# Kernel optimization log

Measured on AMD Instinct MI355X. Metric: run time of the kernel, lower is better.

The kernel has to match this reference:

```python
import jax, jax.numpy as jnp
import numpy as np

B, S, D, H, L = 16, 1024, 512, 8, 32
DH = D // H  # 64


def setup_inputs() -> dict:
    key = jax.random.key(0)
    ks = jax.random.split(key, 12)
    p = lambda k, shape: 0.02 * jax.random.normal(k, shape, jnp.float32)
    return {
        "e_all": jax.random.normal(ks[0], (B, S, D), jnp.float32),
        "e_last": jax.random.normal(ks[1], (1, B, D), jnp.float32),
        "target": jax.random.normal(ks[2], (B, L, 3), jnp.float32),
        "Wq": p(ks[3], (D, D)), "bq": jnp.zeros((D,), jnp.float32),
        "Wk": p(ks[4], (D, D)), "bk": jnp.zeros((D,), jnp.float32),
        "Wv": p(ks[5], (D, D)), "bv": jnp.zeros((D,), jnp.float32),
        "Wo": p(ks[6], (D, D)), "bo": jnp.zeros((D,), jnp.float32),
        "W_ih": p(ks[7], (3 * D, 3 + D)), "W_hh": p(ks[8], (3 * D, D)),
        "b_ih": jnp.zeros((3 * D,), jnp.float32), "b_hh": jnp.zeros((3 * D,), jnp.float32),
        "W_out": p(ks[9], (3, D)), "b_out": jnp.zeros((3,), jnp.float32),
    }


def _forward(e_all, e_last, target, Wq, bq, Wk, bk, Wv, bv, Wo, bo,
             W_ih, W_hh, b_ih, b_hh, W_out, b_out):
    # K/V projections over e_all are loop-invariant in the original python loop;
    # hoist them (identical math). NOTE: the original reshape(B, H, S, DH) on a
    # [B, S, D] tensor is a plain row-major reshape (not a head split) -- kept faithful.
    K = (e_all @ Wk.T + bk).reshape(B, H, S, DH)
    V = (e_all @ Wv.T + bv).reshape(B, H, S, DH)
    h0 = e_last[0]  # [B, D] (single-layer GRU hidden)
    # teacher forcing: step 0 sees zeros, step i sees target[:, i-1]
    d_inputs = jnp.concatenate(
        [jnp.zeros((B, 1, 3), jnp.float32), target[:, :L - 1]], axis=1
    ).transpose(1, 0, 2)  # [L, B, 3]

    def step(h, d_in):
        q = (h @ Wq.T + bq).reshape(B, H, 1, DH)
        # faithful scaling quirk: dim_head ** 1 / 2 == DH / 2
        scores = jnp.einsum('bhqd,bhkd->bhqk', q, K) / (DH / 2)
        dist = jax.nn.softmax(scores, axis=-1)            # [B, H, 1, S]
        attn = jnp.einsum('bhqk,bhkd->bhqd', dist, V).reshape(B, D)
        attn = attn @ Wo.T + bo                           # out projection
        x = jnp.concatenate([attn, d_in], axis=-1)        # [B, D+3]
        gi = x @ W_ih.T + b_ih
        gh = h @ W_hh.T + b_hh
        i_r, i_z, i_n = jnp.split(gi, 3, axis=-1)
        h_r, h_z, h_n = jnp.split(gh, 3, axis=-1)
        r = jax.nn.sigmoid(i_r + h_r)
        z = jax.nn.sigmoid(i_z + h_z)
        n = jnp.tanh(i_n + r * h_n)
        h_new = (1 - z) * n + z * h
        out = h_new @ W_out.T + b_out                     # [B, 3]
        return h_new, (out, dist[:, :, 0, :])

    h_fin, (outs, dists) = jax.lax.scan(step, h0, d_inputs)
    d_outputs = outs.transpose(1, 0, 2)        # [B, L, 3]
    cross_attn = dists.transpose(1, 2, 0, 3)   # [B, H, L, S]
    return d_outputs, h_fin[None, :, :], cross_attn


def reference(e_all, e_last, target, Wq, bq, Wk, bk, Wv, bv, Wo, bo,
              W_ih, W_hh, b_ih, b_hh, W_out, b_out):
    return _forward(e_all, e_last, target, Wq, bq, Wk, bk, Wv, bv, Wo, bo,
                    W_ih, W_hh, b_ih, b_hh, W_out, b_out)
```

## Files before the change

### kernel.cpp

```cpp
#include <hip/hip_runtime.h>
#include <hip/hip_bf16.h>
#include <cstdint>

#define B_  16
#define S_  1024
#define D_  512
#define H_  8
#define L_  32
#define DH_ 64

typedef __attribute__((ext_vector_type(8))) short bf16x8;
typedef __attribute__((ext_vector_type(4))) float f32x4;

__device__ __forceinline__ float bf2f(unsigned short u) {
    union { unsigned int u; float f; } x; x.u = ((unsigned int)u) << 16; return x.f;
}
__device__ __forceinline__ unsigned short f2bf(float f) {
    union { float f; unsigned int u; } x; x.f = f;
    unsigned int r = x.u + 0x7fffu + ((x.u >> 16) & 1u);
    return (unsigned short)(r >> 16);
}

__device__ __forceinline__ void st_dev(float* p, float v) {
    __hip_atomic_store(p, v, __ATOMIC_RELAXED, __HIP_MEMORY_SCOPE_AGENT);
}
__device__ __forceinline__ float ld_dev(const float* p) {
    return __hip_atomic_load(p, __ATOMIC_RELAXED, __HIP_MEMORY_SCOPE_AGENT);
}


__global__ void k_conv(const float* __restrict__ in, unsigned short* __restrict__ out, int n) {
    int i = (blockIdx.x * 256 + threadIdx.x) * 4;
    int stride = gridDim.x * 1024;
    for (; i < n; i += stride) {
        float4 v = *reinterpret_cast<const float4*>(in + i);
        out[i + 0] = f2bf(v.x); out[i + 1] = f2bf(v.y);
        out[i + 2] = f2bf(v.z); out[i + 3] = f2bf(v.w);
    }
}

__global__ void k_transpose_bf(const float* __restrict__ in, unsigned short* __restrict__ out,
                               int R, int C) {
    __shared__ float tile[32][33];
    int c0 = blockIdx.x * 32, r0 = blockIdx.y * 32;
    int tx = threadIdx.x, ty = threadIdx.y;
#pragma unroll
    for (int i = 0; i < 4; i++)
        tile[ty + i * 8][tx] = in[(size_t)(r0 + ty + i * 8) * C + c0 + tx];
    __syncthreads();
#pragma unroll
    for (int i = 0; i < 4; i++)
        out[(size_t)(c0 + ty + i * 8) * R + r0 + tx] = f2bf(tile[tx][ty + i * 8]);
}

__global__ void k_conv_wih(const float* __restrict__ in, unsigned short* __restrict__ out) {
    int i = blockIdx.x * 256 + threadIdx.x;
    int j = i >> 9, k = i & 511;
    out[i] = f2bf(in[j * 515 + k]);
}

__global__ void k_bf_wd(const float* __restrict__ Wih, const float* __restrict__ bih,
                        const float* __restrict__ bo, float* __restrict__ bf_,
                        float* __restrict__ Wd) {
    int j = blockIdx.x * 256 + threadIdx.x;
    if (j >= 1536) return;
    float acc = bih[j];
    for (int k = 0; k < 512; k++) acc += Wih[(size_t)j * 515 + k] * bo[k];
    bf_[j] = acc;
    Wd[j * 3 + 0] = Wih[(size_t)j * 515 + 512];
    Wd[j * 3 + 1] = Wih[(size_t)j * 515 + 513];
    Wd[j * 3 + 2] = Wih[(size_t)j * 515 + 514];
}

__global__ void k_dterm2(const float* __restrict__ target, const float* __restrict__ Wd,
                         const float* __restrict__ bf_, const float* __restrict__ bhh,
                         float* __restrict__ gacc) {
    int i = blockIdx.x * 256 + threadIdx.x;
    int j = i % 3072; int bl = i / 3072; int b = bl % 16; int l = bl / 16;
    float acc;
    if (j < 1536) {
        acc = bf_[j];
        if (l > 0) {
            const float* tg = target + ((size_t)b * L_ + (l - 1)) * 3;
            acc += tg[0] * Wd[j * 3 + 0] + tg[1] * Wd[j * 3 + 1] + tg[2] * Wd[j * 3 + 2];
        }
    } else {
        acc = bhh[j - 1536];
    }
    gacc[i] = acc;
}

template <bool BF16OUT>
__global__ __launch_bounds__(256) void k_gemm_bt(
    const unsigned short* __restrict__ A, const unsigned short* __restrict__ Bm,
    void* __restrict__ Cout, const float* __restrict__ bias, int M, int N, int Kd) {
    __shared__ unsigned short As[128 * 64];
    __shared__ unsigned short Bs[128 * 64];
    const int t = threadIdx.x;
    const int lane = t & 63;
    const int w = t >> 6, wr = w >> 1, wc = w & 1;
    const int m0 = blockIdx.x * 128, n0 = blockIdx.y * 128;
    f32x4 acc[4][4];
#pragma unroll
    for (int i = 0; i < 4; i++)
#pragma unroll
        for (int j = 0; j < 4; j++) acc[i][j] = (f32x4){0.f, 0.f, 0.f, 0.f};

    const int rowt = t >> 3, colt = (t & 7) * 8;
    for (int k0 = 0; k0 < Kd; k0 += 64) {
#pragma unroll
        for (int i = 0; i < 4; i++) {
            int row = i * 32 + rowt;
            __builtin_amdgcn_global_load_lds(
                (const __attribute__((address_space(1))) unsigned int*)(A + (size_t)(m0 + row) * Kd + k0 + colt),
                (__attribute__((address_space(3))) unsigned int*)(As + (i * 256 + t) * 8), 16, 0, 0);
            __builtin_amdgcn_global_load_lds(
                (const __attribute__((address_space(1))) unsigned int*)(Bm + (size_t)(n0 + row) * Kd + k0 + colt),
                (__attribute__((address_space(3))) unsigned int*)(Bs + (i * 256 + t) * 8), 16, 0, 0);
        }
        asm volatile("s_waitcnt vmcnt(0)" ::: "memory");
        __syncthreads();
#pragma unroll
        for (int kk = 0; kk < 2; kk++) {
            bf16x8 af[4], bfr[4];
#pragma unroll
            for (int mi = 0; mi < 4; mi++)
                af[mi] = *reinterpret_cast<const bf16x8*>(
                    As + (wr * 64 + mi * 16 + (lane & 15)) * 64 + kk * 32 + (lane >> 4) * 8);
#pragma unroll
            for (int ni = 0; ni < 4; ni++)
                bfr[ni] = *reinterpret_cast<const bf16x8*>(
                    Bs + (wc * 64 + ni * 16 + (lane & 15)) * 64 + kk * 32 + (lane >> 4) * 8);
#pragma unroll
            for (int mi = 0; mi < 4; mi++)
#pragma unroll
                for (int ni = 0; ni < 4; ni++)
                    acc[mi][ni] = __builtin_amdgcn_mfma_f32_16x16x32_bf16(af[mi], bfr[ni], acc[mi][ni], 0, 0, 0);
        }
        __syncthreads();
    }
    const int rr = (lane >> 4) * 4, cc = lane & 15;
#pragma unroll
    for (int mi = 0; mi < 4; mi++) {
#pragma unroll
        for (int ni = 0; ni < 4; ni++) {
            int col = n0 + wc * 64 + ni * 16 + cc;
            float bv = bias ? bias[col] : 0.f;
            int rowb = m0 + wr * 64 + mi * 16 + rr;
#pragma unroll
            for (int r = 0; r < 4; r++) {
                float v = acc[mi][ni][r] + bv;
                if (BF16OUT) ((unsigned short*)Cout)[(size_t)(rowb + r) * N + col] = f2bf(v);
                else         ((float*)Cout)[(size_t)(rowb + r) * N + col] = v;
            }
        }
    }
}

__device__ __forceinline__ void group_barrier(unsigned* bar, unsigned tgt) {
    asm volatile("s_waitcnt vmcnt(0)" ::: "memory");
    __syncthreads();
    if (threadIdx.x == 0) {
        __hip_atomic_fetch_add(bar, 1u, __ATOMIC_RELAXED, __HIP_MEMORY_SCOPE_AGENT);
        while (__hip_atomic_load(bar, __ATOMIC_RELAXED, __HIP_MEMORY_SCOPE_AGENT) < tgt)
            __builtin_amdgcn_s_sleep(1);
    }
    __syncthreads();
}

__global__ __launch_bounds__(1024, 1) void k_decode(
    const unsigned short* __restrict__ K16, const unsigned short* __restrict__ V16,
    const unsigned short* __restrict__ Wq16, const float* __restrict__ bq,
    const unsigned short* __restrict__ WfT16, const unsigned short* __restrict__ WhhT16,
    float* __restrict__ gacc, float* __restrict__ ssx, const float* __restrict__ e_last,
    const float* __restrict__ Wout, const float* __restrict__ bout,
    float* __restrict__ dout, float* __restrict__ hfin, float* __restrict__ cross,
    unsigned* __restrict__ bars) {
    const int t = threadIdx.x, lane = t & 63, w = t >> 6;
    const int bi = blockIdx.x >> 4, hd = (blockIdx.x >> 1) & 7, sh = blockIdx.x & 1;

    __shared__ char Ks[65536];
    __shared__ char Vs[65536];
    __shared__ float hsh[512];
    __shared__ float qsh[64];
    __shared__ float esh[512];
    __shared__ float red[1024];
    __shared__ float pvred[1024];
    __shared__ float ash[64];
    __shared__ float wred[32];
    __shared__ float sh_ssinv;

    const size_t base = (size_t)bi * (S_ * D_) + (size_t)hd * (S_ * DH_) + (size_t)sh * (512 * 64);

    {
        const int row = t >> 1, half = t & 1;
        const unsigned short* kr = K16 + base + (size_t)row * 64 + half * 32;
        const unsigned short* vr = V16 + base + (size_t)row * 64 + half * 32;
        char* krow = Ks + row * 128;
        char* vrow = Vs + row * 128;
#pragma unroll
        for (int c = 0; c < 4; c++) {
            int slot = half * 4 + c;
            *reinterpret_cast<bf16x8*>(krow + ((slot ^ (row & 7)) * 16)) =
                *reinterpret_cast<const bf16x8*>(kr + c * 8);
            *reinterpret_cast<bf16x8*>(vrow + ((slot ^ (row & 7)) * 16)) =
                *reinterpret_cast<const bf16x8*>(vr + c * 8);
        }
    }
    if (t < 512) hsh[t] = e_last[bi * 512 + t];

    bf16x8 wq[4];
    {
        const unsigned short* wrow = Wq16 + (size_t)(hd * 64 + (t & 63)) * 512 + (t >> 6) * 32;
#pragma unroll
        for (int i = 0; i < 4; i++) wq[i] = *reinterpret_cast<const bf16x8*>(wrow + i * 8);
    }
    __syncthreads();

    for (int l = 0; l < L_; l++) {
        {
            const float* xk = hsh + (t >> 6) * 32;
            float qa = 0.f;
#pragma unroll
            for (int kk = 0; kk < 4; kk++)
#pragma unroll
                for (int e = 0; e < 8; e++)
                    qa += xk[kk * 8 + e] * bf2f((unsigned short)wq[kk][e]);
            red[t] = qa;
        }
        __syncthreads();
        if (t < 64) {
            float s = bq[hd * 64 + t];
#pragma unroll
            for (int p = 0; p < 16; p++) s += red[p * 64 + t];
            qsh[t] = s * (1.f / 32.f);
        }
        __syncthreads();

        {
            const int r = t & 511, kp = t >> 9;
            const char* krow = Ks + r * 128;
            float sc = 0.f;
#pragma unroll
            for (int c = 0; c < 4; c++) {
                int slot = kp * 4 + c;
                bf16x8 kv = *reinterpret_cast<const bf16x8*>(krow + ((slot ^ (r & 7)) * 16));
#pragma unroll
                for (int e = 0; e < 8; e++)
                    sc += qsh[slot * 8 + e] * bf2f((unsigned short)kv[e]);
            }
            red[t] = sc;
        }
        __syncthreads();
        if (t < 512) {
            float e = __expf(red[t] + red[t + 512]);
            esh[t] = e;
            float wsum = e;
#pragma unroll
            for (int off = 1; off < 64; off <<= 1) wsum += __shfl_xor(wsum, off);
            if (lane == 0) wred[w] = wsum;
        }
        __syncthreads();
        if (t == 0) {
            float s = 0.f;
#pragma unroll
            for (int i = 0; i < 8; i++) s += wred[i];
            wred[16] = s;
            st_dev(ssx + (size_t)l * 256 + bi * 16 + hd * 2 + sh, s);
            asm volatile("s_waitcnt vmcnt(0)" ::: "memory");
        }

        {
            const int o = lane & 7, sr8 = lane >> 3;
            float acc[8];
#pragma unroll
            for (int e2 = 0; e2 < 8; e2++) acc[e2] = 0.f;
#pragma unroll
            for (int i = 0; i < 4; i++) {
                int r = w * 32 + sr8 + 8 * i;
                bf16x8 vv = *reinterpret_cast<const bf16x8*>(Vs + r * 128 + ((o ^ (r & 7)) * 16));
                float ev = esh[r];
#pragma unroll
                for (int e2 = 0; e2 < 8; e2++)
                    acc[e2] += ev * bf2f((unsigned short)vv[e2]);
            }
#pragma unroll
            for (int off = 8; off < 64; off <<= 1)
#pragma unroll
                for (int e2 = 0; e2 < 8; e2++)
                    acc[e2] += __shfl_xor(acc[e2], off);
            if (lane < 8) {
#pragma unroll
                for (int e2 = 0; e2 < 8; e2++)
                    pvred[w * 64 + lane * 8 + e2] = acc[e2];
            }
        }
        __syncthreads();

        if (t == 0) {
            const float* sib = ssx + (size_t)l * 256 + bi * 16 + hd * 2 + (sh ^ 1);
            float other;
            while ((other = ld_dev(sib)) == 0.f) __builtin_amdgcn_s_sleep(1);
            sh_ssinv = 1.f / (wred[16] + other);
        }
        __syncthreads();
        const float ssinv = sh_ssinv;
        if (t < 512)
            cross[((size_t)(bi * 8 + hd) * 32 + l) * 1024 + sh * 512 + t] = esh[t] * ssinv;
        if (t < 64) {
            float s = 0.f;
#pragma unroll
            for (int w2 = 0; w2 < 16; w2++) s += pvred[w2 * 64 + t];
            ash[t] = s * ssinv;
        }
        __syncthreads();

        float* g = gacc + ((size_t)l * 16 + bi) * 3072;
        if (t < 768) {
            const unsigned int* wf = (const unsigned int*)WfT16;
            float gi0 = 0.f, gi1 = 0.f;
#pragma unroll 8
            for (int k = 0; k < 64; k++) {
                unsigned int uf = wf[(size_t)(hd * 64 + k) * 768 + t];
                float a = ash[k];
                gi0 += a * bf2f((unsigned short)(uf & 0xffffu));
                gi1 += a * bf2f((unsigned short)(uf >> 16));
            }
            atomicAdd(g + 2 * t, gi0);
            atomicAdd(g + 2 * t + 1, gi1);
        }
        if (t < 384) {
            const unsigned int* wh = (const unsigned int*)WhhT16;
            const int pair = sh * 384 + t;
            float gh0 = 0.f, gh1 = 0.f;
#pragma unroll 8
            for (int k = 0; k < 64; k++) {
                unsigned int uh = wh[(size_t)(hd * 64 + k) * 768 + pair];
                float b = hsh[hd * 64 + k];
                gh0 += b * bf2f((unsigned short)(uh & 0xffffu));
                gh1 += b * bf2f((unsigned short)(uh >> 16));
            }
            atomicAdd(g + 1536 + 2 * pair, gh0);
            atomicAdd(g + 1536 + 2 * pair + 1, gh1);
        }

        group_barrier(bars + bi * 32 + l, 16u);

        float hnew_reg = 0.f;
        if (t < 512) {
            float gi_r = ld_dev(g + t),        gi_z = ld_dev(g + 512 + t),  gi_n = ld_dev(g + 1024 + t);
            float gh_r = ld_dev(g + 1536 + t), gh_z = ld_dev(g + 2048 + t), gh_n = ld_dev(g + 2560 + t);
            float r = 1.f / (1.f + __expf(-(gi_r + gh_r)));
            float z = 1.f / (1.f + __expf(-(gi_z + gh_z)));
            float n = tanhf(gi_n + r * gh_n);
            hnew_reg = (1.f - z) * n + z * hsh[t];
        }
        __syncthreads();
        if (t < 512) hsh[t] = hnew_reg;
        __syncthreads();
        if (hd == 0 && sh == 0) {
            if (t < 512) {
                float hv = hsh[t];
                float p0 = hv * Wout[t], p1 = hv * Wout[512 + t], p2 = hv * Wout[1024 + t];
#pragma unroll
                for (int off = 1; off < 64; off <<= 1) {
                    p0 += __shfl_xor(p0, off);
                    p1 += __shfl_xor(p1, off);
                    p2 += __shfl_xor(p2, off);
                }
                if (lane == 0) { wred[w * 3] = p0; wred[w * 3 + 1] = p1; wred[w * 3 + 2] = p2; }
            }
            __syncthreads();
            if (t < 3) {
                float s = 0.f;
#pragma unroll
                for (int i = 0; i < 8; i++) s += wred[i * 3 + t];
                dout[((size_t)bi * 32 + l) * 3 + t] = s + bout[t];
            }
        }
    }
    if (hd == 0 && sh == 0 && t < 512) hfin[bi * 512 + t] = hsh[t];
}

extern "C" void kernel_launch(void* const* d_in, const int* in_sizes, int n_in,
                              void* d_out, int out_size, void* d_ws, size_t ws_size,
                              hipStream_t stream) {
    (void)in_sizes; (void)n_in; (void)out_size; (void)ws_size;
    const float* e_all  = (const float*)d_in[0];
    const float* e_last = (const float*)d_in[1];
    const float* target = (const float*)d_in[2];
    const float* Wq     = (const float*)d_in[3];
    const float* bq     = (const float*)d_in[4];
    const float* Wk     = (const float*)d_in[5];
    const float* bk     = (const float*)d_in[6];
    const float* Wv     = (const float*)d_in[7];
    const float* bv     = (const float*)d_in[8];
    const float* Wo     = (const float*)d_in[9];
    const float* bo     = (const float*)d_in[10];
    const float* W_ih   = (const float*)d_in[11];
    const float* W_hh   = (const float*)d_in[12];
    const float* b_ih   = (const float*)d_in[13];
    const float* b_hh   = (const float*)d_in[14];
    const float* W_out  = (const float*)d_in[15];
    const float* b_out  = (const float*)d_in[16];
    float* out = (float*)d_out;

    char* ws = (char*)d_ws;
    size_t off = 0;
    auto alloc = [&](size_t bytes) -> void* {
        void* p = ws + off; off += (bytes + 255) & ~(size_t)255; return p;
    };
    unsigned short* eA     = (unsigned short*)alloc(16777216);
    unsigned short* K16    = (unsigned short*)alloc(16777216);
    unsigned short* V16    = (unsigned short*)alloc(16777216);
    unsigned short* Wk16   = (unsigned short*)alloc(524288);
    unsigned short* Wv16   = (unsigned short*)alloc(524288);
    unsigned short* Wq16   = (unsigned short*)alloc(524288);
    unsigned short* WhhT16 = (unsigned short*)alloc(1572864);
    unsigned short* Wih16  = (unsigned short*)alloc(1572864);
    unsigned short* WoT    = (unsigned short*)alloc(524288);
    unsigned short* WfT16  = (unsigned short*)alloc(1572864);
    float* Wf32  = (float*)alloc(3145728);
    float* bf_   = (float*)alloc(6144);
    float* Wd    = (float*)alloc(18432);
    float* gacc  = (float*)alloc(6291456);
    float* ssx   = (float*)alloc(32768);
    unsigned* bars = (unsigned*)alloc(2048);

    float* d_outputs = out;
    float* h_fin     = out + 1536;
    float* cross     = out + 9728;

    hipMemsetAsync(bars, 0, 2048, stream);
    hipMemsetAsync(ssx, 0, 32768, stream);
    k_conv<<<2048, 256, 0, stream>>>(e_all, eA, 8388608);
    k_conv<<<256, 256, 0, stream>>>(Wk, Wk16, 262144);
    k_conv<<<256, 256, 0, stream>>>(Wv, Wv16, 262144);
    k_conv<<<256, 256, 0, stream>>>(Wq, Wq16, 262144);
    k_transpose_bf<<<dim3(16, 48), dim3(32, 8), 0, stream>>>(W_hh, WhhT16, 1536, 512);
    k_transpose_bf<<<dim3(16, 16), dim3(32, 8), 0, stream>>>(Wo, WoT, 512, 512);
    k_conv_wih<<<3072, 256, 0, stream>>>(W_ih, Wih16);
    k_bf_wd<<<6, 256, 0, stream>>>(W_ih, b_ih, bo, bf_, Wd);
    k_dterm2<<<6144, 256, 0, stream>>>(target, Wd, bf_, b_hh, gacc);
    k_gemm_bt<true><<<dim3(128, 4), 256, 0, stream>>>(eA, Wk16, K16, bk, 16384, 512, 512);
    k_gemm_bt<true><<<dim3(128, 4), 256, 0, stream>>>(eA, Wv16, V16, bv, 16384, 512, 512);
    k_gemm_bt<false><<<dim3(12, 4), 256, 0, stream>>>(Wih16, WoT, Wf32, nullptr, 1536, 512, 512);
    k_transpose_bf<<<dim3(16, 48), dim3(32, 8), 0, stream>>>(Wf32, WfT16, 1536, 512);

    k_decode<<<256, 1024, 0, stream>>>(K16, V16, Wq16, bq, WfT16, WhhT16, gacc, ssx, e_last,
                                       W_out, b_out, d_outputs, h_fin, cross, bars);
}
```

Measured before the change: 794.5 us.

## Remove sibling softmax handshake and atomics; defer normalization, precompute next-step hidden gates

Each block now writes its unnormalized softmax partial sum and its gate partials to per-block slots instead of using float atomics. After one group barrier, every block reduces the 16 gi partials, scaling each by its own inverse sum, and the 8 gh partials. This removes the pairwise spin-wait between sibling blocks. The W_hh·h contribution for the next step is computed right after the hidden update, so it is off the critical path before the next barrier. Cross-attention is stored unnormalized and rescaled by a separate k_norm kernel afterward, which adds an extra read-write pass over the attention output and more global loads per step in the reduction.

```diff
diff --git a/kernel.cpp b/kernel.cpp
--- a/kernel.cpp
+++ b/kernel.cpp
@@ -172,12 +172,14 @@
     const unsigned short* __restrict__ K16, const unsigned short* __restrict__ V16,
     const unsigned short* __restrict__ Wq16, const float* __restrict__ bq,
     const unsigned short* __restrict__ WfT16, const unsigned short* __restrict__ WhhT16,
-    float* __restrict__ gacc, float* __restrict__ ssx, const float* __restrict__ e_last,
+    const float* __restrict__ gacc, float* __restrict__ giP, float* __restrict__ ghP,
+    float* __restrict__ ssAll, const float* __restrict__ e_last,
     const float* __restrict__ Wout, const float* __restrict__ bout,
     float* __restrict__ dout, float* __restrict__ hfin, float* __restrict__ cross,
     unsigned* __restrict__ bars) {
     const int t = threadIdx.x, lane = t & 63, w = t >> 6;
     const int bi = blockIdx.x >> 4, hd = (blockIdx.x >> 1) & 7, sh = blockIdx.x & 1;
+    const int p = blockIdx.x & 15;
 
     __shared__ char Ks[65536];
     __shared__ char Vs[65536];
@@ -188,7 +190,7 @@
     __shared__ float pvred[1024];
     __shared__ float ash[64];
     __shared__ float wred[32];
-    __shared__ float sh_ssinv;
+    __shared__ float wred2[16];
 
     const size_t base = (size_t)bi * (S_ * D_) + (size_t)hd * (S_ * DH_) + (size_t)sh * (512 * 64);
 
@@ -217,6 +219,22 @@
     }
     __syncthreads();
 
+    if (t < 384) {
+        const unsigned int* wh = (const unsigned int*)WhhT16;
+        const int pair = sh * 384 + t;
+        float gh0 = 0.f, gh1 = 0.f;
+#pragma unroll 8
+        for (int k = 0; k < 64; k++) {
+            unsigned int uh = wh[(size_t)(hd * 64 + k) * 768 + pair];
+            float b = hsh[hd * 64 + k];
+            gh0 += b * bf2f((unsigned short)(uh & 0xffffu));
+            gh1 += b * bf2f((unsigned short)(uh >> 16));
+        }
+        float* dst = ghP + ((size_t)bi * 8 + hd) * 1536;
+        st_dev(dst + 2 * pair, gh0);
+        st_dev(dst + 2 * pair + 1, gh1);
+    }
+
     for (int l = 0; l < L_; l++) {
         {
             const float* xk = hsh + (t >> 6) * 32;
@@ -232,7 +250,7 @@
         if (t < 64) {
             float s = bq[hd * 64 + t];
 #pragma unroll
-            for (int p = 0; p < 16; p++) s += red[p * 64 + t];
+            for (int pp = 0; pp < 16; pp++) s += red[pp * 64 + t];
             qsh[t] = s * (1.f / 32.f);
         }
         __syncthreads();
@@ -255,6 +273,7 @@
         if (t < 512) {
             float e = __expf(red[t] + red[t + 512]);
             esh[t] = e;
+            cross[((size_t)(bi * 8 + hd) * 32 + l) * 1024 + sh * 512 + t] = e;
             float wsum = e;
 #pragma unroll
             for (int off = 1; off < 64; off <<= 1) wsum += __shfl_xor(wsum, off);
@@ -265,9 +284,7 @@
             float s = 0.f;
 #pragma unroll
             for (int i = 0; i < 8; i++) s += wred[i];
-            wred[16] = s;
-            st_dev(ssx + (size_t)l * 256 + bi * 16 + hd * 2 + sh, s);
-            asm volatile("s_waitcnt vmcnt(0)" ::: "memory");
+            st_dev(ssAll + ((size_t)l * 16 + bi) * 16 + p, s);
         }
 
         {
@@ -296,40 +313,65 @@
             }
         }
         __syncthreads();
-
-        if (t == 0) {
-            const float* sib = ssx + (size_t)l * 256 + bi * 16 + hd * 2 + (sh ^ 1);
-            float other;
-            while ((other = ld_dev(sib)) == 0.f) __builtin_amdgcn_s_sleep(1);
-            sh_ssinv = 1.f / (wred[16] + other);
-        }
-        __syncthreads();
-        const float ssinv = sh_ssinv;
-        if (t < 512)
-            cross[((size_t)(bi * 8 + hd) * 32 + l) * 1024 + sh * 512 + t] = esh[t] * ssinv;
         if (t < 64) {
             float s = 0.f;
 #pragma unroll
             for (int w2 = 0; w2 < 16; w2++) s += pvred[w2 * 64 + t];
-            ash[t] = s * ssinv;
-        }
-        __syncthreads();
-
-        float* g = gacc + ((size_t)l * 16 + bi) * 3072;
-        if (t < 768) {
-            const unsigned int* wf = (const unsigned int*)WfT16;
-            float gi0 = 0.f, gi1 = 0.f;
+            ash[t] = s;
+        }
+        __syncthreads();
+
+        {
+            float* gdst = giP + (((size_t)(l & 1) * 16 + bi) * 16 + p) * 1536;
+            if (t < 768) {
+                const unsigned int* wf = (const unsigned int*)WfT16;
+                float gi0 = 0.f, gi1 = 0.f;
 #pragma unroll 8
-            for (int k = 0; k < 64; k++) {
-                unsigned int uf = wf[(size_t)(hd * 64 + k) * 768 + t];
-                float a = ash[k];
-                gi0 += a * bf2f((unsigned short)(uf & 0xffffu));
-                gi1 += a * bf2f((unsigned short)(uf >> 16));
-            }
-            atomicAdd(g + 2 * t, gi0);
-            atomicAdd(g + 2 * t + 1, gi1);
-        }
-        if (t < 384) {
+                for (int k = 0; k < 64; k++) {
+                    unsigned int uf = wf[(size_t)(hd * 64 + k) * 768 + t];
+                    float a = ash[k];
+                    gi0 += a * bf2f((unsigned short)(uf & 0xffffu));
+                    gi1 += a * bf2f((unsigned short)(uf >> 16));
+                }
+                st_dev(gdst + 2 * t, gi0);
+                st_dev(gdst + 2 * t + 1, gi1);
+            }
+        }
+
+        group_barrier(bars + bi * 32 + l, 16u);
+
+        if (t < 16) wred2[t] = 1.f / ld_dev(ssAll + ((size_t)l * 16 + bi) * 16 + t);
+        __syncthreads();
+        float hnew_reg = 0.f;
+        if (t < 512) {
+            const float* gb = gacc + ((size_t)l * 16 + bi) * 3072;
+            float gr = ld_dev(gb + t), gz = ld_dev(gb + 512 + t), gn = ld_dev(gb + 1024 + t);
+            const float* gp = giP + ((size_t)(l & 1) * 16 + bi) * 16 * 1536;
+#pragma unroll
+            for (int pp = 0; pp < 16; pp++) {
+                float iv = wred2[pp];
+                gr += ld_dev(gp + pp * 1536 + t) * iv;
+                gz += ld_dev(gp + pp * 1536 + 512 + t) * iv;
+                gn += ld_dev(gp + pp * 1536 + 1024 + t) * iv;
+            }
+            float hr = ld_dev(gb + 1536 + t), hz = ld_dev(gb + 2048 + t), hn = ld_dev(gb + 2560 + t);
+            const float* hp = ghP + ((size_t)(l & 1) * 16 + bi) * 8 * 1536;
+#pragma unroll
+            for (int q = 0; q < 8; q++) {
+                hr += ld_dev(hp + q * 1536 + t);
+                hz += ld_dev(hp + q * 1536 + 512 + t);
+                hn += ld_dev(hp + q * 1536 + 1024 + t);
+            }
+            float r = 1.f / (1.f + __expf(-(gr + hr)));
+            float z = 1.f / (1.f + __expf(-(gz + hz)));
+            float n = tanhf(gn + r * hn);
+            hnew_reg = (1.f - z) * n + z * hsh[t];
+        }
+        __syncthreads();
+        if (t < 512) hsh[t] = hnew_reg;
+        __syncthreads();
+
+        if (l < L_ - 1 && t < 384) {
             const unsigned int* wh = (const unsigned int*)WhhT16;
             const int pair = sh * 384 + t;
             float gh0 = 0.f, gh1 = 0.f;
@@ -340,24 +382,11 @@
                 gh0 += b * bf2f((unsigned short)(uh & 0xffffu));
                 gh1 += b * bf2f((unsigned short)(uh >> 16));
             }
-            atomicAdd(g + 1536 + 2 * pair, gh0);
-            atomicAdd(g + 1536 + 2 * pair + 1, gh1);
-        }
-
-        group_barrier(bars + bi * 32 + l, 16u);
-
-        float hnew_reg = 0.f;
-        if (t < 512) {
-            float gi_r = ld_dev(g + t),        gi_z = ld_dev(g + 512 + t),  gi_n = ld_dev(g + 1024 + t);
-            float gh_r = ld_dev(g + 1536 + t), gh_z = ld_dev(g + 2048 + t), gh_n = ld_dev(g + 2560 + t);
-            float r = 1.f / (1.f + __expf(-(gi_r + gh_r)));
-            float z = 1.f / (1.f + __expf(-(gi_z + gh_z)));
-            float n = tanhf(gi_n + r * gh_n);
-            hnew_reg = (1.f - z) * n + z * hsh[t];
-        }
-        __syncthreads();
-        if (t < 512) hsh[t] = hnew_reg;
-        __syncthreads();
+            float* dst = ghP + (((size_t)((l + 1) & 1) * 16 + bi) * 8 + hd) * 1536;
+            st_dev(dst + 2 * pair, gh0);
+            st_dev(dst + 2 * pair + 1, gh1);
+        }
+
         if (hd == 0 && sh == 0) {
             if (t < 512) {
                 float hv = hsh[t];
@@ -380,6 +409,18 @@
         }
     }
     if (hd == 0 && sh == 0 && t < 512) hfin[bi * 512 + t] = hsh[t];
+}
+
+__global__ void k_norm(float* __restrict__ cross, const float* __restrict__ ssAll) {
+    int i = blockIdx.x * 256 + threadIdx.x;
+    size_t b4 = (size_t)i * 4;
+    int bhl = (int)(b4 >> 10);
+    int l = bhl & 31, hd = (bhl >> 5) & 7, bi = bhl >> 8;
+    const float* sp = ssAll + ((size_t)l * 16 + bi) * 16 + hd * 2;
+    float inv = 1.f / (sp[0] + sp[1]);
+    float4 v = *reinterpret_cast<float4*>(cross + b4);
+    v.x *= inv; v.y *= inv; v.z *= inv; v.w *= inv;
+    *reinterpret_cast<float4*>(cross + b4) = v;
 }
 
 extern "C" void kernel_launch(void* const* d_in, const int* in_sizes, int n_in,
@@ -424,7 +465,9 @@
     float* bf_   = (float*)alloc(6144);
     float* Wd    = (float*)alloc(18432);
     float* gacc  = (float*)alloc(6291456);
-    float* ssx   = (float*)alloc(32768);
+    float* giP   = (float*)alloc(3145728);
+    float* ghP   = (float*)alloc(1572864);
+    float* ssAll = (float*)alloc(32768);
     unsigned* bars = (unsigned*)alloc(2048);
 
     float* d_outputs = out;
@@ -432,7 +475,6 @@
     float* cross     = out + 9728;
 
     hipMemsetAsync(bars, 0, 2048, stream);
-    hipMemsetAsync(ssx, 0, 32768, stream);
     k_conv<<<2048, 256, 0, stream>>>(e_all, eA, 8388608);
     k_conv<<<256, 256, 0, stream>>>(Wk, Wk16, 262144);
     k_conv<<<256, 256, 0, stream>>>(Wv, Wv16, 262144);
@@ -447,6 +489,9 @@
     k_gemm_bt<false><<<dim3(12, 4), 256, 0, stream>>>(Wih16, WoT, Wf32, nullptr, 1536, 512, 512);
     k_transpose_bf<<<dim3(16, 48), dim3(32, 8), 0, stream>>>(Wf32, WfT16, 1536, 512);
 
-    k_decode<<<256, 1024, 0, stream>>>(K16, V16, Wq16, bq, WfT16, WhhT16, gacc, ssx, e_last,
-                                       W_out, b_out, d_outputs, h_fin, cross, bars);
-}
+    k_decode<<<256, 1024, 0, stream>>>(K16, V16, Wq16, bq, WfT16, WhhT16, gacc, giP, ghP,
+                                       ssAll, e_last, W_out, b_out, d_outputs, h_fin,
+                                       cross, bars);
+
+    k_norm<<<4096, 256, 0, stream>>>(cross, ssAll);
+}
```

Result: slower. 1.685 ms (+112.1%).
